# Kernel tuning notes

Measured on AMD Instinct MI355X. Metric: run time of the kernel, lower is better.

The kernel has to match this reference:

```python
import jax, jax.numpy as jnp
import numpy as np

BS, SL, D = 4, 2048, 1024
H = 16
HD = D // H  # 64


def setup_inputs() -> dict:
    key = jax.random.key(0)
    ks = jax.random.split(key, 11)
    s = 1.0 / np.sqrt(D)
    inp = {
        "value": jax.random.normal(ks[0], (BS, SL, D), jnp.float32),
        "key_in": jax.random.normal(ks[1], (BS, SL, D), jnp.float32),
        "query": jax.random.normal(ks[2], (BS, SL, D), jnp.float32),
        # nn.Linear weights stored [out, in] (torch convention); orthogonal-ish init approximated by scaled normal
        "Wq": jax.random.normal(ks[3], (D, D), jnp.float32) * s,
        "bq": jax.random.normal(ks[4], (D,), jnp.float32) * 0.01,
        "Wk": jax.random.normal(ks[5], (D, D), jnp.float32) * s,
        "bk": jax.random.normal(ks[6], (D,), jnp.float32) * 0.01,
        "Wv": jax.random.normal(ks[7], (D, D), jnp.float32) * s,
        "bv": jax.random.normal(ks[8], (D,), jnp.float32) * 0.01,
        "Wo": jax.random.normal(ks[9], (D, D), jnp.float32) * s,
        "bo": jax.random.normal(ks[10], (D,), jnp.float32) * 0.01,
    }
    return inp


def reference(value, key_in, query, Wq, bq, Wk, bk, Wv, bv, Wo, bo):
    bs, sl, _ = value.shape
    # projections (torch Linear: x @ W.T + b), then split heads -> [b, h, s, hd]
    def proj(x, W, b):
        return (x @ W.T + b).reshape(bs, -1, H, HD).transpose(0, 2, 1, 3)

    q = proj(query, Wq, bq)
    k = proj(key_in, Wk, bk)
    v = proj(value, Wv, bv)

    scale = 1.0 / jnp.sqrt(jnp.asarray(HD, q.dtype))
    logits = jnp.einsum("bhqd,bhkd->bhqk", q, k) * scale  # [b,h,s,s]
    # amax-subtract + softmax == stable softmax
    attn = jax.nn.softmax(logits, axis=-1)
    out = jnp.einsum("bhqk,bhkd->bhqd", attn, v)
    out = out.transpose(0, 2, 1, 3).reshape(bs, sl, D)  # [b,s,D]
    o = out @ Wo.T + bo
    return o
```

## Files before the change

### kernel.cpp

```cpp
#include <hip/hip_runtime.h>
#include <hip/hip_bf16.h>

typedef __bf16 bf16_t;
typedef __bf16 bf16x8 __attribute__((ext_vector_type(8)));
typedef __bf16 bf16x4 __attribute__((ext_vector_type(4)));
typedef float f32x4 __attribute__((ext_vector_type(4)));
typedef float f32x16 __attribute__((ext_vector_type(16)));

#define BS 4
#define SL 2048
#define DM 1024
#define NH 16
#define HD 64

static __device__ __forceinline__ bf16_t tobf(float x) { return (bf16_t)x; }

#if __has_builtin(__builtin_amdgcn_exp2f)
#define EXP2(x) __builtin_amdgcn_exp2f(x)
#else
#define EXP2(x) exp2f(x)
#endif

#if __has_builtin(__builtin_amdgcn_cvt_pk_bf16_f32)
typedef __bf16 bf16x2_t __attribute__((ext_vector_type(2)));
static __device__ __forceinline__ uint32_t pack_bf16(float a, float b) {
  union { bf16x2_t v; uint32_t u; } c;
  c.v = __builtin_amdgcn_cvt_pk_bf16_f32(a, b);
  return c.u;
}
#else
static __device__ __forceinline__ uint32_t pack_bf16(float a, float b) {
  union { bf16_t e[2]; uint32_t u; } c;
  c.e[0] = tobf(a); c.e[1] = tobf(b);
  return c.u;
}
#endif

static __device__ __forceinline__ void glds16(const void* g, void* l) {
  __builtin_amdgcn_global_load_lds(
      (const __attribute__((address_space(1))) void*)g,
      (__attribute__((address_space(3))) void*)l, 16, 0, 0);
}

__global__ void convert_w_kernel(const float* __restrict__ s0, const float* __restrict__ s1,
                                 const float* __restrict__ s2, const float* __restrict__ s3,
                                 bf16_t* __restrict__ d0, bf16_t* __restrict__ d1,
                                 bf16_t* __restrict__ d2, bf16_t* __restrict__ d3)
{
  const float* s; bf16_t* d;
  switch (blockIdx.y) {
    case 0: s = s0; d = d0; break;
    case 1: s = s1; d = d1; break;
    case 2: s = s2; d = d2; break;
    default: s = s3; d = d3; break;
  }
  int i = (blockIdx.x * 256 + threadIdx.x) * 4;
  float4 v = *(const float4*)(s + i);
  bf16x4 o; o[0] = tobf(v.x); o[1] = tobf(v.y); o[2] = tobf(v.z); o[3] = tobf(v.w);
  *(bf16x4*)(d + i) = o;
}

__global__ __launch_bounds__(256, 2) void gemm_qkv_kernel(
    const float* __restrict__ Aq, const float* __restrict__ Ak, const float* __restrict__ Avv,
    const bf16_t* __restrict__ Wcat,
    const float* __restrict__ bq, const float* __restrict__ bk, const float* __restrict__ bvv,
    bf16_t* __restrict__ Qb, bf16_t* __restrict__ Kbo, bf16_t* __restrict__ Vtb)
{
  __shared__ __align__(16) char sMem[49152];

  const int proj = blockIdx.y >> 3;
  const float* Af   = proj == 0 ? Aq : (proj == 1 ? Ak : Avv);
  const float* bias = proj == 0 ? bq : (proj == 1 ? bk : bvv);

  const int tid  = threadIdx.x;
  const int wave = tid >> 6;
  const int lane = tid & 63;
  const int l15  = lane & 15;
  const int quad = lane >> 4;
  const int m0 = blockIdx.x * 128;
  const int nW = blockIdx.y * 128;
  const int n0 = (blockIdx.y & 7) * 128;
  const int wm = (wave & 1) * 64;
  const int wn = (wave >> 1) * 64;

  auto stage = [&](int r, int k0) {
    char* base = sMem + r * 24576;
#pragma unroll
    for (int t = 0; t < 4; t++) {
      int slot = wave * 4 + t;
      int f = slot * 64 + lane;
      int row = f >> 3;
      int cg = (f & 7) ^ (row & 7);
      glds16(Af + (size_t)(m0 + row) * DM + k0 + cg * 4, base + slot * 1024);
    }
#pragma unroll
    for (int t = 0; t < 2; t++) {
      int slot = wave * 2 + t;
      int f = slot * 64 + lane;
      int row = f >> 2;
      int cg = (f & 3) ^ (row & 3);
      glds16(Wcat + (size_t)(nW + row) * DM + k0 + cg * 8, base + 16384 + slot * 1024);
    }
  };

  f32x4 acc[4][4];
#pragma unroll
  for (int i = 0; i < 4; i++)
#pragma unroll
    for (int j = 0; j < 4; j++) acc[i][j] = f32x4{0.f, 0.f, 0.f, 0.f};

  stage(0, 0);
  for (int t = 0; t < 32; ++t) {
    __syncthreads();
    if (t < 31) stage((t + 1) & 1, (t + 1) * 32);

    const float*  sA = (const float*)(sMem + (t & 1) * 24576);
    const bf16_t* sB = (const bf16_t*)(sMem + (t & 1) * 24576 + 16384);

    bf16x8 af[4], bfr[4];
#pragma unroll
    for (int i = 0; i < 4; i++) {
      int row = wm + i * 16 + l15;
      int sw = row & 7;
      const float* base = sA + row * 32;
      f32x4 lo = *(const f32x4*)(base + (((quad * 2)     ^ sw) * 4));
      f32x4 hi = *(const f32x4*)(base + (((quad * 2 + 1) ^ sw) * 4));
      bf16x8 o;
      o[0] = tobf(lo[0]); o[1] = tobf(lo[1]); o[2] = tobf(lo[2]); o[3] = tobf(lo[3]);
      o[4] = tobf(hi[0]); o[5] = tobf(hi[1]); o[6] = tobf(hi[2]); o[7] = tobf(hi[3]);
      af[i] = o;
    }
#pragma unroll
    for (int j = 0; j < 4; j++) {
      int row = wn + j * 16 + l15;
      bfr[j] = *(const bf16x8*)(sB + row * 32 + (quad ^ (row & 3)) * 8);
    }

#pragma unroll
    for (int i = 0; i < 4; i++)
#pragma unroll
      for (int j = 0; j < 4; j++)
        acc[i][j] = __builtin_amdgcn_mfma_f32_16x16x32_bf16(af[i], bfr[j], acc[i][j], 0, 0, 0);
  }

  if (proj < 2) {
    bf16_t* C = proj == 0 ? Qb : Kbo;
#pragma unroll
    for (int j = 0; j < 4; j++) {
      int col = n0 + wn + j * 16 + l15;
      float bv = bias[col];
#pragma unroll
      for (int i = 0; i < 4; i++) {
        int rowb = m0 + wm + i * 16 + quad * 4;
#pragma unroll
        for (int r = 0; r < 4; r++)
          C[(size_t)(rowb + r) * DM + col] = tobf(acc[i][j][r] + bv);
      }
    }
  } else {
#pragma unroll
    for (int j = 0; j < 4; j++) {
      int col = n0 + wn + j * 16 + l15;
      float bv = bias[col];
      int head = col >> 6, hd = col & 63;
#pragma unroll
      for (int i = 0; i < 4; i++) {
        int rowb = m0 + wm + i * 16 + quad * 4;
        int b = rowb >> 11, s = rowb & (SL - 1);
        bf16x4 o;
#pragma unroll
        for (int r = 0; r < 4; r++) o[r] = tobf(acc[i][j][r] + bv);
        *(bf16x4*)(Vtb + ((size_t)(b * NH + head) * HD + hd) * SL + s) = o;
      }
    }
  }
}

__global__ __launch_bounds__(256, 2) void gemm_out_kernel(
    const bf16_t* __restrict__ A, const bf16_t* __restrict__ Bw,
    const float* __restrict__ bias, float* __restrict__ C)
{
  __shared__ __align__(16) char sMem[32768];

  const int tid  = threadIdx.x;
  const int wave = tid >> 6;
  const int lane = tid & 63;
  const int l15  = lane & 15;
  const int quad = lane >> 4;
  const int m0 = blockIdx.x * 128;
  const int n0 = blockIdx.y * 128;
  const int wm = (wave & 1) * 64;
  const int wn = (wave >> 1) * 64;

  auto stage = [&](int r, int k0) {
    char* base = sMem + r * 16384;
#pragma unroll
    for (int t = 0; t < 2; t++) {
      int slot = wave * 2 + t;
      int f = slot * 64 + lane;
      int row = f >> 2;
      int cg = (f & 3) ^ (row & 3);
      glds16(A  + (size_t)(m0 + row) * DM + k0 + cg * 8, base + slot * 1024);
      glds16(Bw + (size_t)(n0 + row) * DM + k0 + cg * 8, base + 8192 + slot * 1024);
    }
  };

  f32x4 acc[4][4];
#pragma unroll
  for (int i = 0; i < 4; i++)
#pragma unroll
    for (int j = 0; j < 4; j++) acc[i][j] = f32x4{0.f, 0.f, 0.f, 0.f};

  stage(0, 0);
  for (int t = 0; t < 32; ++t) {
    __syncthreads();
    if (t < 31) stage((t + 1) & 1, (t + 1) * 32);

    const bf16_t* sA = (const bf16_t*)(sMem + (t & 1) * 16384);
    const bf16_t* sB = sA + 4096;

    bf16x8 af[4], bfr[4];
#pragma unroll
    for (int i = 0; i < 4; i++) {
      int row = wm + i * 16 + l15;
      af[i] = *(const bf16x8*)(sA + row * 32 + (quad ^ (row & 3)) * 8);
    }
#pragma unroll
    for (int j = 0; j < 4; j++) {
      int row = wn + j * 16 + l15;
      bfr[j] = *(const bf16x8*)(sB + row * 32 + (quad ^ (row & 3)) * 8);
    }

#pragma unroll
    for (int i = 0; i < 4; i++)
#pragma unroll
      for (int j = 0; j < 4; j++)
        acc[i][j] = __builtin_amdgcn_mfma_f32_16x16x32_bf16(af[i], bfr[j], acc[i][j], 0, 0, 0);
  }

#pragma unroll
  for (int j = 0; j < 4; j++) {
    int col = n0 + wn + j * 16 + l15;
    float bv = bias[col];
#pragma unroll
    for (int i = 0; i < 4; i++) {
      int rowb = m0 + wm + i * 16 + quad * 4;
#pragma unroll
      for (int r = 0; r < 4; r++)
        C[(size_t)(rowb + r) * DM + col] = acc[i][j][r] + bv;
    }
  }
}

__global__ __launch_bounds__(256, 4) void attn_kernel(
    const bf16_t* __restrict__ Q, const bf16_t* __restrict__ Kb,
    const bf16_t* __restrict__ Vt, bf16_t* __restrict__ O)
{
  __shared__ __align__(16) char sMem[32768];

  const int tid  = threadIdx.x;
  const int wave = tid >> 6;
  const int lane = tid & 63;
  const int l31  = lane & 31;
  const int h    = lane >> 5;
  const int swl  = l31 & 7;

  const int id  = blockIdx.x;
  const int xcd = id & 7, slot = id >> 3;
  const int bh  = xcd * 8 + (slot >> 4);
  const int qi  = slot & 15;
  const int b = bh >> 4, hh = bh & 15;
  const int q0 = qi * 128 + wave * 32;

  auto stage = [&](int r, int k0) {
    char* base = sMem + r * 16384;
#pragma unroll
    for (int t = 0; t < 2; t++) {
      int slot2 = wave * 2 + t;
      int f = slot2 * 64 + lane;
      int row = f >> 3;
      int cg = (f & 7) ^ ((row + (row >> 3)) & 7);
      glds16(Kb + (size_t)(b * SL + k0 + row) * DM + hh * HD + cg * 8,
             base + slot2 * 1024);
      glds16(Vt + ((size_t)bh * HD + row) * SL + k0 + cg * 8,
             base + 8192 + slot2 * 1024);
    }
  };

  bf16x8 qf[4];
  {
    const bf16_t* qp = Q + (size_t)(b * SL + q0 + l31) * DM + hh * HD + h * 8;
#pragma unroll
    for (int c = 0; c < 4; c++) {
      bf16x8 v = *(const bf16x8*)(qp + c * 16);
#pragma unroll
      for (int j = 0; j < 8; j++) v[j] = tobf((float)v[j] * 0.18033688f);
      qf[c] = v;
    }
  }

  f32x16 o_acc[2];
#pragma unroll
  for (int m = 0; m < 2; m++)
#pragma unroll
    for (int r = 0; r < 16; r++) o_acc[m][r] = 0.f;
  float rs0 = 0.f, rs1 = 0.f;

  stage(0, 0);
  for (int t = 0; t < 32; ++t) {
    __syncthreads();
    if (t < 31) stage((t + 1) & 1, (t + 1) * 64);

    const bf16_t* sK = (const bf16_t*)(sMem + (t & 1) * 16384);
    const bf16_t* sV = sK + 4096;

#pragma unroll
    for (int s = 0; s < 2; s++) {
      int rowK = s * 32 + l31;
      int kkK = (rowK + (rowK >> 3)) & 7;
      bf16x8 kf[4];
#pragma unroll
      for (int c = 0; c < 4; c++)
        kf[c] = *(const bf16x8*)(sK + rowK * 64 + (((c * 2 + h) ^ kkK) * 8));

      f32x16 st;
#pragma unroll
      for (int r = 0; r < 16; r++) st[r] = -17.312340f;
#pragma unroll
      for (int c = 0; c < 4; c++)
        st = __builtin_amdgcn_mfma_f32_32x32x16_bf16(kf[c], qf[c], st, 0, 0, 0);

      uint32_t w[8];
#pragma unroll
      for (int i = 0; i < 8; i++) {
        float p0 = EXP2(st[2 * i]);
        float p1 = EXP2(st[2 * i + 1]);
        rs0 += p0; rs1 += p1;
        w[i] = pack_bf16(p0, p1);
      }
      uint32_t y0 = (uint32_t)__shfl_xor((int)(h ? w[0] : w[2]), 32);
      uint32_t y1 = (uint32_t)__shfl_xor((int)(h ? w[1] : w[3]), 32);
      uint32_t y2 = (uint32_t)__shfl_xor((int)(h ? w[4] : w[6]), 32);
      uint32_t y3 = (uint32_t)__shfl_xor((int)(h ? w[5] : w[7]), 32);
      union { uint32_t u[4]; bf16x8 v; } pf0, pf1;
      pf0.u[0] = h ? y0   : w[0];
      pf0.u[1] = h ? y1   : w[1];
      pf0.u[2] = h ? w[2] : y0;
      pf0.u[3] = h ? w[3] : y1;
      pf1.u[0] = h ? y2   : w[4];
      pf1.u[1] = h ? y3   : w[5];
      pf1.u[2] = h ? w[6] : y2;
      pf1.u[3] = h ? w[7] : y3;

#pragma unroll
      for (int m = 0; m < 2; m++) {
        int rowV = m * 32 + l31;
        int kkV = (rowV + (rowV >> 3)) & 7;
#pragma unroll
        for (int c = 0; c < 2; c++) {
          int chunk = (s * 4 + c * 2 + h) ^ kkV;
          bf16x8 vf = *(const bf16x8*)(sV + rowV * 64 + chunk * 8);
          o_acc[m] = __builtin_amdgcn_mfma_f32_32x32x16_bf16(
              vf, (c ? pf1.v : pf0.v), o_acc[m], 0, 0, 0);
        }
      }
    }
  }

  float rs = rs0 + rs1;
  rs += __shfl_xor(rs, 32);
  float inv = 1.f / rs;
  bf16_t* so = (bf16_t*)sMem + wave * 2048;
#pragma unroll
  for (int m = 0; m < 2; m++) {
#pragma unroll
    for (int r = 0; r < 16; r++) {
      int hd = m * 32 + (r & 3) + 8 * (r >> 2) + 4 * h;
      so[l31 * 64 + (((hd >> 3) ^ swl) * 8) + (hd & 7)] = tobf(o_acc[m][r] * inv);
    }
  }
  asm volatile("s_waitcnt lgkmcnt(0)" ::: "memory");
  {
    int qr = lane >> 1, hf = lane & 1;
    int sw2 = qr & 7;
#pragma unroll
    for (int cc = 0; cc < 4; cc++) {
      int chunk = (hf * 4 + cc) ^ sw2;
      bf16x8 v = *(const bf16x8*)(so + qr * 64 + chunk * 8);
      *(bf16x8*)(O + (size_t)(b * SL + q0 + qr) * DM + hh * HD + hf * 32 + cc * 8) = v;
    }
  }
}

extern "C" void kernel_launch(void* const* d_in, const int* in_sizes, int n_in,
                              void* d_out, int out_size, void* d_ws, size_t ws_size,
                              hipStream_t stream)
{
  const float* value  = (const float*)d_in[0];
  const float* key_in = (const float*)d_in[1];
  const float* query  = (const float*)d_in[2];
  const float* Wq = (const float*)d_in[3];
  const float* bq = (const float*)d_in[4];
  const float* Wk = (const float*)d_in[5];
  const float* bk = (const float*)d_in[6];
  const float* Wv = (const float*)d_in[7];
  const float* bv = (const float*)d_in[8];
  const float* Wo = (const float*)d_in[9];
  const float* bo = (const float*)d_in[10];

  char* ws = (char*)d_ws;
  const size_t sz  = (size_t)BS * SL * DM * sizeof(bf16_t);
  const size_t wsz = (size_t)DM * DM * sizeof(bf16_t);
  bf16_t* Qb   = (bf16_t*)(ws + 0 * sz);
  bf16_t* Kb   = (bf16_t*)(ws + 1 * sz);
  bf16_t* Ob   = (bf16_t*)(ws + 2 * sz);
  bf16_t* Vtb  = (bf16_t*)(ws + 3 * sz);
  bf16_t* Wcat = (bf16_t*)(ws + 4 * sz);
  bf16_t* Wob  = (bf16_t*)(ws + 4 * sz + 3 * wsz);

  const int M = BS * SL;

  convert_w_kernel<<<dim3(1024, 4), 256, 0, stream>>>(
      Wq, Wk, Wv, Wo, Wcat, Wcat + DM * DM, Wcat + 2 * DM * DM, Wob);

  gemm_qkv_kernel<<<dim3(M / 128, 24), 256, 0, stream>>>(
      query, key_in, value, Wcat, bq, bk, bv, Qb, Kb, Vtb);

  attn_kernel<<<dim3(SL / 128 * BS * NH), 256, 0, stream>>>(Qb, Kb, Vtb, Ob);

  gemm_out_kernel<<<dim3(M / 128, DM / 128), 256, 0, stream>>>(Ob, Wob, bo, (float*)d_out);
}
```

Before: 354.9 us.

## Convert fp32 A tiles to bf16 in registers before storing to LDS in QKV GEMM

The QKV projection GEMM now loads the fp32 activation tile into registers, converts it to bf16, and writes it to LDS after the MFMA loop, replacing the direct global-to-LDS copy of fp32 data and the per-fragment conversion. This halves the LDS footprint and LDS read traffic for A and removes the repeated conversions. The trade-off is register staging of the prefetch, since global loads for A now go through VGPRs, which adds latency exposure and register pressure. A dead stageB lambda is left in place.

Result: no change. 349.5 us (-1.5%).

```diff
diff --git a/kernel.cpp b/kernel.cpp
--- a/kernel.cpp
+++ b/kernel.cpp
@@ -66,7 +66,7 @@
     const float* __restrict__ bq, const float* __restrict__ bk, const float* __restrict__ bvv,
     bf16_t* __restrict__ Qb, bf16_t* __restrict__ Kbo, bf16_t* __restrict__ Vtb)
 {
-  __shared__ __align__(16) char sMem[49152];
+  __shared__ __align__(16) char sMem[32768];
 
   const int proj = blockIdx.y >> 3;
   const float* Af   = proj == 0 ? Aq : (proj == 1 ? Ak : Avv);
@@ -83,23 +83,51 @@
   const int wm = (wave & 1) * 64;
   const int wn = (wave >> 1) * 64;
 
-  auto stage = [&](int r, int k0) {
-    char* base = sMem + r * 24576;
-#pragma unroll
-    for (int t = 0; t < 4; t++) {
-      int slot = wave * 4 + t;
-      int f = slot * 64 + lane;
-      int row = f >> 3;
-      int cg = (f & 7) ^ (row & 7);
-      glds16(Af + (size_t)(m0 + row) * DM + k0 + cg * 4, base + slot * 1024);
-    }
+  auto stageB = [&](int r, int k0) {
+    char* base = sMem + r * 16384 + 8192;
 #pragma unroll
     for (int t = 0; t < 2; t++) {
       int slot = wave * 2 + t;
       int f = slot * 64 + lane;
       int row = f >> 2;
       int cg = (f & 3) ^ (row & 3);
-      glds16(Wcat + (size_t)(nW + row) * DM + k0 + cg * 8, base + 16384 + slot * 1024);
+      glds16(Wcat + (size_t)(nW + row) * DM + k0 + cg * 8, base + 16384 - 8192 + slot * 1024 - 8192);
+    }
+  };
+  (void)stageB;
+
+  f32x4 aLo[2], aHi[2];
+  auto loadA = [&](int k0) {
+#pragma unroll
+    for (int t2 = 0; t2 < 2; t2++) {
+      int f = t2 * 256 + tid;
+      int row = f >> 2, c = f & 3;
+      const float* p = Af + (size_t)(m0 + row) * DM + k0 + c * 8;
+      aLo[t2] = *(const f32x4*)p;
+      aHi[t2] = *(const f32x4*)(p + 4);
+    }
+  };
+  auto writeA = [&](int r) {
+    char* base = sMem + r * 16384;
+#pragma unroll
+    for (int t2 = 0; t2 < 2; t2++) {
+      int f = t2 * 256 + tid;
+      int row = f >> 2, c = f & 3;
+      bf16x8 o;
+#pragma unroll
+      for (int j = 0; j < 4; j++) { o[j] = tobf(aLo[t2][j]); o[4 + j] = tobf(aHi[t2][j]); }
+      *(bf16x8*)(base + row * 64 + ((c ^ (row & 3)) * 16)) = o;
+    }
+  };
+  auto stageBv = [&](int r, int k0) {
+    char* base = sMem + r * 16384 + 8192;
+#pragma unroll
+    for (int t = 0; t < 2; t++) {
+      int slot = wave * 2 + t;
+      int f = slot * 64 + lane;
+      int row = f >> 2;
+      int cg = (f & 3) ^ (row & 3);
+      glds16(Wcat + (size_t)(nW + row) * DM + k0 + cg * 8, base + slot * 1024);
     }
   };
 
@@ -109,26 +137,24 @@
 #pragma unroll
     for (int j = 0; j < 4; j++) acc[i][j] = f32x4{0.f, 0.f, 0.f, 0.f};
 
-  stage(0, 0);
+  loadA(0);
+  stageBv(0, 0);
+  writeA(0);
   for (int t = 0; t < 32; ++t) {
     __syncthreads();
-    if (t < 31) stage((t + 1) & 1, (t + 1) * 32);
-
-    const float*  sA = (const float*)(sMem + (t & 1) * 24576);
-    const bf16_t* sB = (const bf16_t*)(sMem + (t & 1) * 24576 + 16384);
+    if (t < 31) {
+      loadA((t + 1) * 32);
+      stageBv((t + 1) & 1, (t + 1) * 32);
+    }
+
+    const bf16_t* sA = (const bf16_t*)(sMem + (t & 1) * 16384);
+    const bf16_t* sB = sA + 4096;
 
     bf16x8 af[4], bfr[4];
 #pragma unroll
     for (int i = 0; i < 4; i++) {
       int row = wm + i * 16 + l15;
-      int sw = row & 7;
-      const float* base = sA + row * 32;
-      f32x4 lo = *(const f32x4*)(base + (((quad * 2)     ^ sw) * 4));
-      f32x4 hi = *(const f32x4*)(base + (((quad * 2 + 1) ^ sw) * 4));
-      bf16x8 o;
-      o[0] = tobf(lo[0]); o[1] = tobf(lo[1]); o[2] = tobf(lo[2]); o[3] = tobf(lo[3]);
-      o[4] = tobf(hi[0]); o[5] = tobf(hi[1]); o[6] = tobf(hi[2]); o[7] = tobf(hi[3]);
-      af[i] = o;
+      af[i] = *(const bf16x8*)(sA + row * 32 + (quad ^ (row & 3)) * 8);
     }
 #pragma unroll
     for (int j = 0; j < 4; j++) {
@@ -141,6 +167,8 @@
 #pragma unroll
       for (int j = 0; j < 4; j++)
         acc[i][j] = __builtin_amdgcn_mfma_f32_16x16x32_bf16(af[i], bfr[j], acc[i][j], 0, 0, 0);
+
+    if (t < 31) writeA((t + 1) & 1);
   }
 
   if (proj < 2) {
```

## Pre-convert activations to bf16 and rewrite QKV GEMM as 256x256 pipelined tile

Applied to the files above, without the earlier changes.

Adds a separate kernel that converts the fp32 query/key/value activations to bf16 in workspace. The QKV GEMM then works on bf16 A only and moves to 512 threads with 256x256 tiles. It uses a 4-deep LDS ring fed by global_load_lds, manual vmcnt waits and barriers, and raised wave priority around the MFMA bursts. This removes the fp32 LDS traffic and in-loop conversion and improves data reuse. In exchange it adds an extra full pass that reads and writes the activations, plus a 128KB LDS footprint that limits occupancy.

Measured after the change: 359.3 us. Within noise of the previous version (+1.2%).

```diff
diff --git a/kernel.cpp b/kernel.cpp
--- a/kernel.cpp
+++ b/kernel.cpp
@@ -42,6 +42,12 @@
       (__attribute__((address_space(3))) void*)l, 16, 0, 0);
 }
 
+#define BAR()    asm volatile("s_barrier" ::: "memory")
+#define WAITV0() asm volatile("s_waitcnt vmcnt(0)" ::: "memory")
+#define WAITV4() asm volatile("s_waitcnt vmcnt(4)" ::: "memory")
+#define WAITLG() asm volatile("s_waitcnt lgkmcnt(0)" ::: "memory")
+#define SCHEDB() __builtin_amdgcn_sched_barrier(0)
+
 __global__ void convert_w_kernel(const float* __restrict__ s0, const float* __restrict__ s1,
                                  const float* __restrict__ s2, const float* __restrict__ s3,
                                  bf16_t* __restrict__ d0, bf16_t* __restrict__ d1,
@@ -60,117 +66,151 @@
   *(bf16x4*)(d + i) = o;
 }
 
-__global__ __launch_bounds__(256, 2) void gemm_qkv_kernel(
-    const float* __restrict__ Aq, const float* __restrict__ Ak, const float* __restrict__ Avv,
-    const bf16_t* __restrict__ Wcat,
+__global__ void convert_a_kernel(const float* __restrict__ q, const float* __restrict__ k,
+                                 const float* __restrict__ v, bf16_t* __restrict__ dst)
+{
+  const float* s = blockIdx.y == 0 ? q : (blockIdx.y == 1 ? k : v);
+  bf16_t* d = dst + (size_t)blockIdx.y * ((size_t)BS * SL * DM);
+  int i = (blockIdx.x * 256 + threadIdx.x) * 4;
+  float4 x = *(const float4*)(s + i);
+  bf16x4 o; o[0] = tobf(x.x); o[1] = tobf(x.y); o[2] = tobf(x.z); o[3] = tobf(x.w);
+  *(bf16x4*)(d + i) = o;
+}
+
+__global__ __launch_bounds__(512, 2) void gemm_qkv_kernel(
+    const bf16_t* __restrict__ Aall, const bf16_t* __restrict__ Wcat,
     const float* __restrict__ bq, const float* __restrict__ bk, const float* __restrict__ bvv,
     bf16_t* __restrict__ Qb, bf16_t* __restrict__ Kbo, bf16_t* __restrict__ Vtb)
 {
-  __shared__ __align__(16) char sMem[49152];
-
-  const int proj = blockIdx.y >> 3;
-  const float* Af   = proj == 0 ? Aq : (proj == 1 ? Ak : Avv);
-  const float* bias = proj == 0 ? bq : (proj == 1 ? bk : bvv);
+  __shared__ __align__(16) char sMem[131072];
 
   const int tid  = threadIdx.x;
   const int wave = tid >> 6;
   const int lane = tid & 63;
   const int l15  = lane & 15;
   const int quad = lane >> 4;
-  const int m0 = blockIdx.x * 128;
-  const int nW = blockIdx.y * 128;
-  const int n0 = (blockIdx.y & 7) * 128;
-  const int wm = (wave & 1) * 64;
-  const int wn = (wave >> 1) * 64;
-
-  auto stage = [&](int r, int k0) {
-    char* base = sMem + r * 24576;
-#pragma unroll
-    for (int t = 0; t < 4; t++) {
-      int slot = wave * 4 + t;
-      int f = slot * 64 + lane;
-      int row = f >> 3;
-      int cg = (f & 7) ^ (row & 7);
-      glds16(Af + (size_t)(m0 + row) * DM + k0 + cg * 4, base + slot * 1024);
-    }
-#pragma unroll
-    for (int t = 0; t < 2; t++) {
-      int slot = wave * 2 + t;
+  const int wr   = wave >> 2;
+  const int wc   = wave & 3;
+  const int m0 = blockIdx.x * 256;
+  const int nTile = blockIdx.y;
+  const int proj = nTile >> 2;
+  const int n0 = (nTile & 3) * 256;
+  const int nW = nTile * 256;
+
+  const bf16_t* Af = Aall + (size_t)proj * ((size_t)BS * SL * DM);
+  const float* bias = proj == 0 ? bq : (proj == 1 ? bk : bvv);
+
+  auto stageA = [&](int u) {
+    int tu = u >> 1, kk = u & 1;
+    char* dst = sMem + (u & 3) * 16384;
+#pragma unroll
+    for (int g2 = 0; g2 < 2; g2++) {
+      int slot = wave * 2 + g2;
       int f = slot * 64 + lane;
       int row = f >> 2;
       int cg = (f & 3) ^ (row & 3);
-      glds16(Wcat + (size_t)(nW + row) * DM + k0 + cg * 8, base + 16384 + slot * 1024);
+      glds16(Af + (size_t)(m0 + row) * DM + tu * 64 + kk * 32 + cg * 8,
+             dst + slot * 1024);
     }
   };
-
-  f32x4 acc[4][4];
-#pragma unroll
-  for (int i = 0; i < 4; i++)
+  auto stageB = [&](int u) {
+    int tu = u >> 1, kk = u & 1;
+    char* dst = sMem + 65536 + (u & 3) * 16384;
+#pragma unroll
+    for (int g2 = 0; g2 < 2; g2++) {
+      int slot = wave * 2 + g2;
+      int f = slot * 64 + lane;
+      int row = f >> 2;
+      int cg = (f & 3) ^ (row & 3);
+      glds16(Wcat + (size_t)(nW + row) * DM + tu * 64 + kk * 32 + cg * 8,
+             dst + slot * 1024);
+    }
+  };
+
+  f32x4 acc[8][4];
+#pragma unroll
+  for (int i = 0; i < 8; i++)
 #pragma unroll
     for (int j = 0; j < 4; j++) acc[i][j] = f32x4{0.f, 0.f, 0.f, 0.f};
 
-  stage(0, 0);
-  for (int t = 0; t < 32; ++t) {
-    __syncthreads();
-    if (t < 31) stage((t + 1) & 1, (t + 1) * 32);
-
-    const float*  sA = (const float*)(sMem + (t & 1) * 24576);
-    const bf16_t* sB = (const bf16_t*)(sMem + (t & 1) * 24576 + 16384);
-
-    bf16x8 af[4], bfr[4];
-#pragma unroll
-    for (int i = 0; i < 4; i++) {
-      int row = wm + i * 16 + l15;
-      int sw = row & 7;
-      const float* base = sA + row * 32;
-      f32x4 lo = *(const f32x4*)(base + (((quad * 2)     ^ sw) * 4));
-      f32x4 hi = *(const f32x4*)(base + (((quad * 2 + 1) ^ sw) * 4));
-      bf16x8 o;
-      o[0] = tobf(lo[0]); o[1] = tobf(lo[1]); o[2] = tobf(lo[2]); o[3] = tobf(lo[3]);
-      o[4] = tobf(hi[0]); o[5] = tobf(hi[1]); o[6] = tobf(hi[2]); o[7] = tobf(hi[3]);
-      af[i] = o;
-    }
-#pragma unroll
-    for (int j = 0; j < 4; j++) {
-      int row = wn + j * 16 + l15;
-      bfr[j] = *(const bf16x8*)(sB + row * 32 + (quad ^ (row & 3)) * 8);
-    }
-
-#pragma unroll
-    for (int i = 0; i < 4; i++)
-#pragma unroll
-      for (int j = 0; j < 4; j++)
-        acc[i][j] = __builtin_amdgcn_mfma_f32_16x16x32_bf16(af[i], bfr[j], acc[i][j], 0, 0, 0);
+  stageA(0); stageB(0); stageA(1); stageB(1); stageA(2); stageB(2);
+  WAITV4(); SCHEDB();
+  BAR();
+
+  bf16x8 b[4];
+  for (int T = 0; T < 16; ++T) {
+#pragma unroll
+    for (int p = 0; p < 4; ++p) {
+      const int qm = p & 1, kk = p >> 1;
+      const int ubuf = (2 * T + kk) & 3;
+      const char* ab = sMem + ubuf * 16384;
+      const char* bb = sMem + 65536 + ubuf * 16384;
+
+      bf16x8 a[4];
+#pragma unroll
+      for (int mf = 0; mf < 4; mf++) {
+        int row = wr * 128 + qm * 64 + mf * 16 + l15;
+        a[mf] = *(const bf16x8*)(ab + row * 64 + ((quad ^ (row & 3)) * 16));
+      }
+      if (qm == 0) {
+#pragma unroll
+        for (int nf = 0; nf < 4; nf++) {
+          int row = wc * 64 + nf * 16 + l15;
+          b[nf] = *(const bf16x8*)(bb + row * 64 + ((quad ^ (row & 3)) * 16));
+        }
+      }
+
+      if (p == 0)      { int u = 2 * T + 3; if (u < 32) stageA(u); }
+      else if (p == 1) { int u = 2 * T + 3; if (u < 32) stageB(u); }
+      else if (p == 2) { int u = 2 * T + 4; if (u < 32) stageA(u); }
+      else             { int u = 2 * T + 4; if (u < 32) stageB(u); }
+
+      if (p == 3 && T < 15) {
+        if (T == 14) { WAITV0(); } else { WAITV4(); }
+        SCHEDB();
+      }
+      BAR();
+      WAITLG(); SCHEDB();
+      __builtin_amdgcn_s_setprio(1);
+#pragma unroll
+      for (int mf = 0; mf < 4; mf++)
+#pragma unroll
+        for (int nf = 0; nf < 4; nf++)
+          acc[qm * 4 + mf][nf] = __builtin_amdgcn_mfma_f32_16x16x32_bf16(
+              a[mf], b[nf], acc[qm * 4 + mf][nf], 0, 0, 0);
+      __builtin_amdgcn_s_setprio(0);
+      BAR();
+    }
   }
 
   if (proj < 2) {
     bf16_t* C = proj == 0 ? Qb : Kbo;
 #pragma unroll
-    for (int j = 0; j < 4; j++) {
-      int col = n0 + wn + j * 16 + l15;
+    for (int nf = 0; nf < 4; nf++) {
+      int col = n0 + wc * 64 + nf * 16 + l15;
       float bv = bias[col];
 #pragma unroll
-      for (int i = 0; i < 4; i++) {
-        int rowb = m0 + wm + i * 16 + quad * 4;
+      for (int i = 0; i < 8; i++) {
+        int rowb = m0 + wr * 128 + (i >> 2) * 64 + (i & 3) * 16 + quad * 4;
 #pragma unroll
         for (int r = 0; r < 4; r++)
-          C[(size_t)(rowb + r) * DM + col] = tobf(acc[i][j][r] + bv);
+          C[(size_t)(rowb + r) * DM + col] = tobf(acc[i][nf][r] + bv);
       }
     }
   } else {
 #pragma unroll
-    for (int j = 0; j < 4; j++) {
-      int col = n0 + wn + j * 16 + l15;
+    for (int nf = 0; nf < 4; nf++) {
+      int col = n0 + wc * 64 + nf * 16 + l15;
       float bv = bias[col];
       int head = col >> 6, hd = col & 63;
 #pragma unroll
-      for (int i = 0; i < 4; i++) {
-        int rowb = m0 + wm + i * 16 + quad * 4;
-        int b = rowb >> 11, s = rowb & (SL - 1);
+      for (int i = 0; i < 8; i++) {
+        int rowb = m0 + wr * 128 + (i >> 2) * 64 + (i & 3) * 16 + quad * 4;
+        int bidx = rowb >> 11, s = rowb & (SL - 1);
         bf16x4 o;
 #pragma unroll
-        for (int r = 0; r < 4; r++) o[r] = tobf(acc[i][j][r] + bv);
-        *(bf16x4*)(Vtb + ((size_t)(b * NH + head) * HD + hd) * SL + s) = o;
+        for (int r = 0; r < 4; r++) o[r] = tobf(acc[i][nf][r] + bv);
+        *(bf16x4*)(Vtb + ((size_t)(bidx * NH + head) * HD + hd) * SL + s) = o;
       }
     }
   }
@@ -417,14 +457,18 @@
   bf16_t* Vtb  = (bf16_t*)(ws + 3 * sz);
   bf16_t* Wcat = (bf16_t*)(ws + 4 * sz);
   bf16_t* Wob  = (bf16_t*)(ws + 4 * sz + 3 * wsz);
+  bf16_t* Abf  = (bf16_t*)(ws + 4 * sz + 4 * wsz);
 
   const int M = BS * SL;
 
   convert_w_kernel<<<dim3(1024, 4), 256, 0, stream>>>(
       Wq, Wk, Wv, Wo, Wcat, Wcat + DM * DM, Wcat + 2 * DM * DM, Wob);
 
-  gemm_qkv_kernel<<<dim3(M / 128, 24), 256, 0, stream>>>(
-      query, key_in, value, Wcat, bq, bk, bv, Qb, Kb, Vtb);
+  convert_a_kernel<<<dim3(M * DM / 1024, 3), 256, 0, stream>>>(
+      query, key_in, value, Abf);
+
+  gemm_qkv_kernel<<<dim3(M / 256, 12), 512, 0, stream>>>(
+      Abf, Wcat, bq, bk, bv, Qb, Kb, Vtb);
 
   attn_kernel<<<dim3(SL / 128 * BS * NH), 256, 0, stream>>>(Qb, Kb, Vtb, Ob);
 
```
